# Kernel optimization log

Hardware: AMD Instinct MI355X
Metric: run time of the kernel (lower is better)

The kernel has to match this reference:

```python
import jax, jax.numpy as jnp
import numpy as np

B, L, T = 256, 256, 50  # batch, max_len, num_tags


def setup_inputs() -> dict:
    key = jax.random.key(0)
    k1, k2, k3 = jax.random.split(key, 3)
    feats = jax.random.normal(k1, (B, L, T), dtype=jnp.float32)
    trans_m = jax.random.normal(k2, (T, T), dtype=jnp.float32)
    tags = jax.random.randint(k3, (B, L), 0, T)
    mask = jnp.ones((B, L), dtype=jnp.int32)
    return {"feats": feats, "trans_m": trans_m, "tags": tags, "mask": mask}


def _normalizer(logits, trans_m, m):
    # logits: (L, B, T), m: (L, B) float mask
    alpha0 = logits[0]  # (B, T)

    def step(alpha, inp):
        emit, mt = inp  # (B, T), (B,)
        # (B, T_from, T_to) broadcast add, logsumexp over T_from
        tmp = alpha[:, :, None] + trans_m[None, :, :] + emit[:, None, :]
        new = jax.nn.logsumexp(tmp, axis=1)
        alpha = jnp.where(mt[:, None] > 0, new, alpha)
        return alpha, None

    alpha, _ = jax.lax.scan(step, alpha0, (logits[1:], m[1:]))
    return jax.nn.logsumexp(alpha, axis=1)  # (B,)


def _gold_score(logits, trans_m, tags_t, m):
    # logits: (L, B, T); tags_t: (L, B); m: (L, B)
    trans_sc = trans_m[tags_t[:-1], tags_t[1:]] * m[1:]  # (L-1, B)
    emit_sc = jnp.take_along_axis(logits, tags_t[:, :, None], axis=2)[..., 0] * m  # (L, B)
    return jnp.sum(trans_sc + emit_sc[:-1], axis=0) + emit_sc[-1]  # (B,)


def reference(feats, trans_m, tags, mask):
    # feats: (B, L, T) -> (L, B, T); include_start_end_trans=False
    logits = jnp.transpose(feats, (1, 0, 2))
    tags_t = tags.T
    m = mask.T.astype(feats.dtype)
    all_path = _normalizer(logits, trans_m, m)
    gold = _gold_score(logits, trans_m, tags_t, m)
    return all_path - gold  # (B,) loss per example
```

## Files before the change

kernel.cpp:

```cpp
#include <hip/hip_runtime.h>
#include <math.h>


#define TAGS 50
#define LEN 256
#define NB 256
#define HALF 128
#define INV_LN2 1.4426950408889634f
#define LN2 0.6931471805599453f

typedef __attribute__((ext_vector_type(8))) short bf16x8;
typedef __attribute__((ext_vector_type(4))) float f32x4;

#if __has_builtin(__builtin_amdgcn_exp2f)
#define EXP2F(x) __builtin_amdgcn_exp2f(x)
#else
#define EXP2F(x) exp2f(x)
#endif
#if __has_builtin(__builtin_amdgcn_logf)
#define LOG2F(x) __builtin_amdgcn_logf(x)
#else
#define LOG2F(x) log2f(x)
#endif
#if __has_builtin(__builtin_amdgcn_rcpf)
#define RCPF(x) __builtin_amdgcn_rcpf(x)
#else
#define RCPF(x) (1.0f / (x))
#endif

__device__ __forceinline__ float readlane_f(float v, int srclane) {
  return __builtin_bit_cast(float,
      __builtin_amdgcn_readlane(__builtin_bit_cast(int, v), srclane));
}

__device__ __forceinline__ int bf16pair(float lo, float hi) {
  unsigned lb = (__builtin_bit_cast(unsigned, lo) + 0x8000u) >> 16;
  unsigned hb = (__builtin_bit_cast(unsigned, hi) + 0x8000u) & 0xFFFF0000u;
  return (int)(hb | lb);
}

union U8 { int i[4]; bf16x8 v; };

#define WS_U(b)  ((b) * 64)
#define WS_W(b)  ((NB + (b)) * 64)
#define WS_SF(b) (2 * NB * 64 + (b))
#define WS_SB(b) (2 * NB * 64 + NB + (b))

__global__ __launch_bounds__(64) void crf_scan_kernel(
    const float* __restrict__ feats,
    const float* __restrict__ trans,
    const int*   __restrict__ mask,
    float*       __restrict__ ws)
{
  const int bid    = blockIdx.x;
  const bool is_fwd = bid < NB;
  const int b      = is_fwd ? bid : bid - NB;
  const int lane   = threadIdx.x;
  const int q      = lane >> 4;
  const int n      = lane & 15;

  __shared__ __align__(16) float fraw[HALF * TAGS];
  __shared__ __align__(16) float flexp[HALF * 64];
  __shared__ int ml[HALF];

  const int base_l = is_fwd ? 0 : HALF;
  const float* fb = feats + ((size_t)b * LEN + base_l) * TAGS;
  const int*   mb = mask + b * LEN + base_l;

  {
    const float4* fv = (const float4*)fb;
    for (int i = lane; i < (HALF * TAGS) / 4; i += 64) {
      float4 v4 = fv[i];
      v4.x *= INV_LN2; v4.y *= INV_LN2; v4.z *= INV_LN2; v4.w *= INV_LN2;
      *(float4*)&fraw[i * 4] = v4;
    }
    for (int i = lane; i < HALF; i += 64) ml[i] = mb[i];
  }
  __syncthreads();

  for (int l = 0; l < HALF; ++l) {
    float v = 0.0f;
    if (lane < TAGS) v = EXP2F(fraw[l * TAGS + lane]);
    flexp[l * 64 + lane] = v;
  }
  __syncthreads();

  U8 Afr[4][2];
#pragma unroll
  for (int t = 0; t < 4; ++t)
#pragma unroll
    for (int c = 0; c < 2; ++c)
#pragma unroll
      for (int r = 0; r < 4; ++r) {
        const int col = 16 * t + n;
        const int tag0 = 16 * c + 4 * q + r;
        const int tag1 = tag0 + 32;
        float e0 = 0.0f, e1 = 0.0f;
        if (col < TAGS) {
          if (tag0 < TAGS)
            e0 = EXP2F((is_fwd ? trans[tag0 * TAGS + col]
                               : trans[col * TAGS + tag0]) * INV_LN2);
          if (tag1 < TAGS)
            e1 = EXP2F((is_fwd ? trans[tag1 * TAGS + col]
                               : trans[col * TAGS + tag1]) * INV_LN2);
        }
        Afr[t][c].i[r] = bf16pair(e0, e1);
      }

  const f32x4 zero4 = {0.0f, 0.0f, 0.0f, 0.0f};

#define LDEH(l_, I_) (*(const f32x4*)&flexp[(l_) * 64 + 16 * (I_) + 4 * q])

  float va[16];
  float S;

  if (is_fwd) {
    const float r0 = RCPF(flexp[0]);
    {
      f32x4 i0 = LDEH(0, 0), i1 = LDEH(0, 1), i2 = LDEH(0, 2), i3 = LDEH(0, 3);
#pragma unroll
      for (int r = 0; r < 4; ++r) {
        va[r]      = i0[r] * r0;
        va[4 + r]  = i1[r] * r0;
        va[8 + r]  = i2[r] * r0;
        va[12 + r] = i3[r] * r0;
      }
    }
    S = fraw[0];

    f32x4 eh0 = LDEH(1, 0), eh1 = LDEH(1, 1), eh2 = LDEH(1, 2), eh3 = LDEH(1, 3);
    int m_nxt = ml[1];

#pragma unroll 2
    for (int l = 1; l < HALF; ++l) {
      const int m_cur = m_nxt;
      const int ln = (l + 1 < HALF) ? (l + 1) : (HALF - 1);

      const float cc = readlane_f(va[0], 0);
      const float rr = RCPF(cc);

      U8 B0, B1;
#pragma unroll
      for (int r = 0; r < 4; ++r) {
        B0.i[r] = bf16pair(va[r],     va[8 + r]);
        B1.i[r] = bf16pair(va[4 + r], va[12 + r]);
      }

      f32x4 d0 = __builtin_amdgcn_mfma_f32_16x16x32_bf16(Afr[0][1].v, B1.v, zero4, 0, 0, 0);
      f32x4 d1 = __builtin_amdgcn_mfma_f32_16x16x32_bf16(Afr[1][1].v, B1.v, zero4, 0, 0, 0);
      f32x4 d2 = __builtin_amdgcn_mfma_f32_16x16x32_bf16(Afr[2][1].v, B1.v, zero4, 0, 0, 0);
      f32x4 d3 = __builtin_amdgcn_mfma_f32_16x16x32_bf16(Afr[3][1].v, B1.v, zero4, 0, 0, 0);
      d0 = __builtin_amdgcn_mfma_f32_16x16x32_bf16(Afr[0][0].v, B0.v, d0, 0, 0, 0);
      d1 = __builtin_amdgcn_mfma_f32_16x16x32_bf16(Afr[1][0].v, B0.v, d1, 0, 0, 0);
      d2 = __builtin_amdgcn_mfma_f32_16x16x32_bf16(Afr[2][0].v, B0.v, d2, 0, 0, 0);
      d3 = __builtin_amdgcn_mfma_f32_16x16x32_bf16(Afr[3][0].v, B0.v, d3, 0, 0, 0);

      f32x4 en0 = LDEH(ln, 0), en1 = LDEH(ln, 1), en2 = LDEH(ln, 2), en3 = LDEH(ln, 3);
      const int m_n2 = ml[ln];

#pragma unroll
      for (int r = 0; r < 4; ++r) {
        va[r]      = ((m_cur > 0) ? d0[r] * eh0[r] : va[r])      * rr;
        va[4 + r]  = ((m_cur > 0) ? d1[r] * eh1[r] : va[4 + r])  * rr;
        va[8 + r]  = ((m_cur > 0) ? d2[r] * eh2[r] : va[8 + r])  * rr;
        va[12 + r] = ((m_cur > 0) ? d3[r] * eh3[r] : va[12 + r]) * rr;
      }
      S += LOG2F(cc);
      eh0 = en0; eh1 = en1; eh2 = en2; eh3 = en3;
      m_nxt = m_n2;
    }

    if (n == 0) {
#pragma unroll
      for (int I = 0; I < 4; ++I)
#pragma unroll
        for (int r = 0; r < 4; ++r)
          ws[WS_U(b) + 16 * I + 4 * q + r] = va[4 * I + r];
    }
    if (lane == 0) ws[WS_SF(b)] = S;
  } else {
#pragma unroll
    for (int I = 0; I < 4; ++I)
#pragma unroll
      for (int r = 0; r < 4; ++r)
        va[4 * I + r] = (16 * I + 4 * q + r < TAGS) ? 1.0f : 0.0f;
    S = 0.0f;

    f32x4 eh0 = LDEH(HALF - 1, 0), eh1 = LDEH(HALF - 1, 1),
          eh2 = LDEH(HALF - 1, 2), eh3 = LDEH(HALF - 1, 3);
    int m_nxt = ml[HALF - 1];

#pragma unroll 2
    for (int l = HALF - 1; l >= 0; --l) {
      const int m_cur = m_nxt;
      const int ln = (l > 0) ? (l - 1) : 0;

      const float cc = readlane_f(va[0], 0);
      const float rr = RCPF(cc);

      float x[16];
#pragma unroll
      for (int r = 0; r < 4; ++r) {
        x[r]      = va[r]      * eh0[r];
        x[4 + r]  = va[4 + r]  * eh1[r];
        x[8 + r]  = va[8 + r]  * eh2[r];
        x[12 + r] = va[12 + r] * eh3[r];
      }

      U8 B0, B1;
#pragma unroll
      for (int r = 0; r < 4; ++r) {
        B0.i[r] = bf16pair(x[r],     x[8 + r]);
        B1.i[r] = bf16pair(x[4 + r], x[12 + r]);
      }

      f32x4 d0 = __builtin_amdgcn_mfma_f32_16x16x32_bf16(Afr[0][1].v, B1.v, zero4, 0, 0, 0);
      f32x4 d1 = __builtin_amdgcn_mfma_f32_16x16x32_bf16(Afr[1][1].v, B1.v, zero4, 0, 0, 0);
      f32x4 d2 = __builtin_amdgcn_mfma_f32_16x16x32_bf16(Afr[2][1].v, B1.v, zero4, 0, 0, 0);
      f32x4 d3 = __builtin_amdgcn_mfma_f32_16x16x32_bf16(Afr[3][1].v, B1.v, zero4, 0, 0, 0);
      d0 = __builtin_amdgcn_mfma_f32_16x16x32_bf16(Afr[0][0].v, B0.v, d0, 0, 0, 0);
      d1 = __builtin_amdgcn_mfma_f32_16x16x32_bf16(Afr[1][0].v, B0.v, d1, 0, 0, 0);
      d2 = __builtin_amdgcn_mfma_f32_16x16x32_bf16(Afr[2][0].v, B0.v, d2, 0, 0, 0);
      d3 = __builtin_amdgcn_mfma_f32_16x16x32_bf16(Afr[3][0].v, B0.v, d3, 0, 0, 0);

      f32x4 en0 = LDEH(ln, 0), en1 = LDEH(ln, 1), en2 = LDEH(ln, 2), en3 = LDEH(ln, 3);
      const int m_n2 = ml[ln];

#pragma unroll
      for (int r = 0; r < 4; ++r) {
        va[r]      = ((m_cur > 0) ? d0[r] : va[r])      * rr;
        va[4 + r]  = ((m_cur > 0) ? d1[r] : va[4 + r])  * rr;
        va[8 + r]  = ((m_cur > 0) ? d2[r] : va[8 + r])  * rr;
        va[12 + r] = ((m_cur > 0) ? d3[r] : va[12 + r]) * rr;
      }
      S += LOG2F(cc);
      eh0 = en0; eh1 = en1; eh2 = en2; eh3 = en3;
      m_nxt = m_n2;
    }

    if (n == 0) {
#pragma unroll
      for (int I = 0; I < 4; ++I)
#pragma unroll
        for (int r = 0; r < 4; ++r)
          ws[WS_W(b) + 16 * I + 4 * q + r] = va[4 * I + r];
    }
    if (lane == 0) ws[WS_SB(b)] = S;
  }
#undef LDEH
}

__global__ __launch_bounds__(64) void crf_combine_kernel(
    const float* __restrict__ feats,
    const float* __restrict__ trans,
    const int*   __restrict__ tags,
    const int*   __restrict__ mask,
    const float* __restrict__ ws,
    float*       __restrict__ out)
{
  const int b = blockIdx.x;
  const int lane = threadIdx.x;

  float s = ws[WS_U(b) + lane] * ws[WS_W(b) + lane];
#pragma unroll
  for (int off = 32; off; off >>= 1) s += __shfl_xor(s, off, 64);

  const float* fb = feats + (size_t)b * (LEN * TAGS);
  const int*   tb = tags + b * LEN;
  const int*   mb = mask + b * LEN;
  float gp = 0.0f;
#pragma unroll
  for (int k = 0; k < 4; ++k) {
    const int p = lane + 64 * k;
    const int tg = tb[p];
    if (mb[p] > 0) {
      float vv = fb[p * TAGS + tg];
      if (p >= 1) vv += trans[tb[p - 1] * TAGS + tg];
      gp += vv;
    }
  }
#pragma unroll
  for (int off = 32; off; off >>= 1) gp += __shfl_xor(gp, off, 64);

  if (lane == 0) {
    const float Sf = ws[WS_SF(b)];
    const float Sb = ws[WS_SB(b)];
    out[b] = LN2 * (Sf + Sb + LOG2F(s)) - gp;
  }
}

extern "C" void kernel_launch(void* const* d_in, const int* in_sizes, int n_in,
                              void* d_out, int out_size, void* d_ws, size_t ws_size,
                              hipStream_t stream) {
  const float* feats = (const float*)d_in[0];
  const float* trans = (const float*)d_in[1];
  const int*   tags  = (const int*)d_in[2];
  const int*   mask  = (const int*)d_in[3];
  float* out = (float*)d_out;
  float* ws  = (float*)d_ws;

  crf_scan_kernel<<<2 * NB, 64, 0, stream>>>(feats, trans, mask, ws);
  crf_combine_kernel<<<NB, 64, 0, stream>>>(feats, trans, tags, mask, ws, out);
}
```

Measured before the change: 116.8 us.

## Split CRF scan into eight parallel segment transfer-matrix products per batch

Replaces the forward/backward two-kernel scheme with a single 512-thread block per sequence. Each of eight waves computes a 32-step segment transfer matrix (64x64) with MFMA, and the segments are then chained on one wave through LDS as vector-matrix products. The gold-path score is computed in the same block, so the workspace round trip and the second launch go away. The cost is 4x more MFMA work per step, since each step now multiplies a full matrix instead of a vector. The intermediate matrices are also stored in bf16, which may reduce accuracy.

```diff
diff --git a/kernel.cpp b/kernel.cpp
--- a/kernel.cpp
+++ b/kernel.cpp
@@ -5,12 +5,13 @@
 #define TAGS 50
 #define LEN 256
 #define NB 256
-#define HALF 128
+#define TOTF (NB * LEN * TAGS)
 #define INV_LN2 1.4426950408889634f
 #define LN2 0.6931471805599453f
 
 typedef __attribute__((ext_vector_type(8))) short bf16x8;
 typedef __attribute__((ext_vector_type(4))) float f32x4;
+typedef __attribute__((ext_vector_type(4), aligned(4))) float f32x4u;
 
 #if __has_builtin(__builtin_amdgcn_exp2f)
 #define EXP2F(x) __builtin_amdgcn_exp2f(x)
@@ -33,57 +34,49 @@
       __builtin_amdgcn_readlane(__builtin_bit_cast(int, v), srclane));
 }
 
-__device__ __forceinline__ int bf16pair(float lo, float hi) {
+__device__ __forceinline__ int bf16pairInit(float lo, float hi) {
   unsigned lb = (__builtin_bit_cast(unsigned, lo) + 0x8000u) >> 16;
   unsigned hb = (__builtin_bit_cast(unsigned, hi) + 0x8000u) & 0xFFFF0000u;
   return (int)(hb | lb);
 }
 
+__device__ __forceinline__ float bf16f(unsigned short u) {
+  return __builtin_bit_cast(float, ((unsigned)u) << 16);
+}
+
+#define PACK2(dst, lo, hi) \
+  asm("v_cvt_pk_bf16_f32 %0, %1, %2" : "=v"(dst) : "v"(lo), "v"(hi))
+
 union U8 { int i[4]; bf16x8 v; };
 
-#define WS_U(b)  ((b) * 64)
-#define WS_W(b)  ((NB + (b)) * 64)
-#define WS_SF(b) (2 * NB * 64 + (b))
-#define WS_SB(b) (2 * NB * 64 + NB + (b))
-
-__global__ __launch_bounds__(64) void crf_scan_kernel(
+__global__ __launch_bounds__(512, 1) void crf_seg_kernel(
     const float* __restrict__ feats,
     const float* __restrict__ trans,
+    const int*   __restrict__ tags,
     const int*   __restrict__ mask,
-    float*       __restrict__ ws)
+    float*       __restrict__ out)
 {
-  const int bid    = blockIdx.x;
-  const bool is_fwd = bid < NB;
-  const int b      = is_fwd ? bid : bid - NB;
-  const int lane   = threadIdx.x;
-  const int q      = lane >> 4;
-  const int n      = lane & 15;
-
-  __shared__ __align__(16) float fraw[HALF * TAGS];
-  __shared__ __align__(16) float flexp[HALF * 64];
-  __shared__ int ml[HALF];
-
-  const int base_l = is_fwd ? 0 : HALF;
-  const float* fb = feats + ((size_t)b * LEN + base_l) * TAGS;
-  const int*   mb = mask + b * LEN + base_l;
-
-  {
-    const float4* fv = (const float4*)fb;
-    for (int i = lane; i < (HALF * TAGS) / 4; i += 64) {
-      float4 v4 = fv[i];
-      v4.x *= INV_LN2; v4.y *= INV_LN2; v4.z *= INV_LN2; v4.w *= INV_LN2;
-      *(float4*)&fraw[i * 4] = v4;
-    }
-    for (int i = lane; i < HALF; i += 64) ml[i] = mb[i];
-  }
-  __syncthreads();
-
-  for (int l = 0; l < HALF; ++l) {
-    float v = 0.0f;
-    if (lane < TAGS) v = EXP2F(fraw[l * TAGS + lane]);
-    flexp[l * 64 + lane] = v;
-  }
-  __syncthreads();
+  const int b    = blockIdx.x;
+  const int tid  = threadIdx.x;
+  const int w    = tid >> 6;
+  const int lane = tid & 63;
+  const int q    = lane >> 4;
+  const int n    = lane & 15;
+
+  __shared__ __align__(16) unsigned short Plds[6][64][64];
+  __shared__ __align__(16) float u_lds[64];
+  __shared__ __align__(16) float w_lds[64];
+  __shared__ float Sseg[8];
+  __shared__ float norm_s, gold_s;
+
+  const int* mbp = mask + b * LEN;
+  const unsigned long long mb0 = __ballot(mbp[lane] > 0);
+  const unsigned long long mb1 = __ballot(mbp[64 + lane] > 0);
+  const unsigned long long mb2 = __ballot(mbp[128 + lane] > 0);
+  const unsigned long long mb3 = __ballot(mbp[192 + lane] > 0);
+#define MASKBIT(L)                                                          \
+  ((int)(((((L) & 128) ? (((L) & 64) ? mb3 : mb2)                           \
+                       : (((L) & 64) ? mb1 : mb0)) >> ((L) & 63)) & 1ull))
 
   U8 Afr[4][2];
 #pragma unroll
@@ -97,196 +90,218 @@
         const int tag1 = tag0 + 32;
         float e0 = 0.0f, e1 = 0.0f;
         if (col < TAGS) {
-          if (tag0 < TAGS)
-            e0 = EXP2F((is_fwd ? trans[tag0 * TAGS + col]
-                               : trans[col * TAGS + tag0]) * INV_LN2);
-          if (tag1 < TAGS)
-            e1 = EXP2F((is_fwd ? trans[tag1 * TAGS + col]
-                               : trans[col * TAGS + tag1]) * INV_LN2);
+          if (tag0 < TAGS) e0 = EXP2F(trans[tag0 * TAGS + col] * INV_LN2);
+          if (tag1 < TAGS) e1 = EXP2F(trans[tag1 * TAGS + col] * INV_LN2);
         }
-        Afr[t][c].i[r] = bf16pair(e0, e1);
+        Afr[t][c].i[r] = bf16pairInit(e0, e1);
       }
 
   const f32x4 zero4 = {0.0f, 0.0f, 0.0f, 0.0f};
 
-#define LDEH(l_, I_) (*(const f32x4*)&flexp[(l_) * 64 + 16 * (I_) + 4 * q])
-
-  float va[16];
-  float S;
-
-  if (is_fwd) {
-    const float r0 = RCPF(flexp[0]);
-    {
-      f32x4 i0 = LDEH(0, 0), i1 = LDEH(0, 1), i2 = LDEH(0, 2), i3 = LDEH(0, 3);
-#pragma unroll
-      for (int r = 0; r < 4; ++r) {
-        va[r]      = i0[r] * r0;
-        va[4 + r]  = i1[r] * r0;
-        va[8 + r]  = i2[r] * r0;
-        va[12 + r] = i3[r] * r0;
+  f32x4 d[4][4];
+#pragma unroll
+  for (int J = 0; J < 4; ++J)
+#pragma unroll
+    for (int I = 0; I < 4; ++I)
+#pragma unroll
+      for (int r = 0; r < 4; ++r)
+        d[J][I][r] = (16 * J + n == 16 * I + 4 * q + r) ? 1.0f : 0.0f;
+
+  const int l0 = 32 * w + 1;
+  float S = 0.0f;
+  f32x4u rA[4], rB[4];
+
+#define LOADG(BK, L) do {                                                   \
+    const float* _p = feats + (size_t)b * (LEN * TAGS) + (size_t)(L) * TAGS;\
+    BK[0] = *(const f32x4u*)(_p + 4 * q);                                   \
+    BK[1] = *(const f32x4u*)(_p + 16 + 4 * q);                              \
+    BK[2] = *(const f32x4u*)(_p + 32 + 4 * q);                              \
+    const float* _p3 = _p + 46 + 4 * q;                                     \
+    const float* _lim = feats + (TOTF - 4);                                 \
+    if (_p3 > _lim) _p3 = _lim;                                             \
+    BK[3] = *(const f32x4u*)_p3;                                            \
+  } while (0)
+
+#define RENORMM() do {                                                      \
+    const float _cc = readlane_f(d[0][0][0], 0);                            \
+    const float _rr = RCPF(_cc);                                            \
+    S += LOG2F(_cc);                                                        \
+    _Pragma("unroll") for (int _J = 0; _J < 4; ++_J)                        \
+    _Pragma("unroll") for (int _I = 0; _I < 4; ++_I)                        \
+    _Pragma("unroll") for (int _r = 0; _r < 4; ++_r)                        \
+      d[_J][_I][_r] *= _rr;                                                 \
+  } while (0)
+
+#define STEPM(EH, L) do {                                                   \
+    if (MASKBIT(L)) {                                                       \
+      float ev[4][4];                                                       \
+      _Pragma("unroll") for (int _i = 0; _i < 3; ++_i)                      \
+      _Pragma("unroll") for (int _r = 0; _r < 4; ++_r)                      \
+        ev[_i][_r] = EXP2F(EH[_i][_r] * INV_LN2);                           \
+      ev[3][0] = EXP2F(EH[3][2] * INV_LN2);                                 \
+      ev[3][1] = EXP2F(EH[3][3] * INV_LN2);                                 \
+      ev[3][2] = 0.0f; ev[3][3] = 0.0f;                                     \
+      _Pragma("unroll") for (int _J = 0; _J < 4; ++_J) {                    \
+        U8 B0, B1;                                                          \
+        _Pragma("unroll") for (int _r = 0; _r < 4; ++_r) {                  \
+          PACK2(B0.i[_r], d[_J][0][_r], d[_J][2][_r]);                      \
+          PACK2(B1.i[_r], d[_J][1][_r], d[_J][3][_r]);                      \
+        }                                                                   \
+        f32x4 t0 = __builtin_amdgcn_mfma_f32_16x16x32_bf16(Afr[0][1].v, B1.v, zero4, 0, 0, 0); \
+        f32x4 t1 = __builtin_amdgcn_mfma_f32_16x16x32_bf16(Afr[1][1].v, B1.v, zero4, 0, 0, 0); \
+        f32x4 t2 = __builtin_amdgcn_mfma_f32_16x16x32_bf16(Afr[2][1].v, B1.v, zero4, 0, 0, 0); \
+        f32x4 t3 = __builtin_amdgcn_mfma_f32_16x16x32_bf16(Afr[3][1].v, B1.v, zero4, 0, 0, 0); \
+        t0 = __builtin_amdgcn_mfma_f32_16x16x32_bf16(Afr[0][0].v, B0.v, t0, 0, 0, 0); \
+        t1 = __builtin_amdgcn_mfma_f32_16x16x32_bf16(Afr[1][0].v, B0.v, t1, 0, 0, 0); \
+        t2 = __builtin_amdgcn_mfma_f32_16x16x32_bf16(Afr[2][0].v, B0.v, t2, 0, 0, 0); \
+        t3 = __builtin_amdgcn_mfma_f32_16x16x32_bf16(Afr[3][0].v, B0.v, t3, 0, 0, 0); \
+        _Pragma("unroll") for (int _r = 0; _r < 4; ++_r) {                  \
+          d[_J][0][_r] = t0[_r] * ev[0][_r];                                \
+          d[_J][1][_r] = t1[_r] * ev[1][_r];                                \
+          d[_J][2][_r] = t2[_r] * ev[2][_r];                                \
+          d[_J][3][_r] = t3[_r] * ev[3][_r];                                \
+        }                                                                   \
+      }                                                                     \
+    }                                                                       \
+  } while (0)
+
+  LOADG(rA, l0);
+  LOADG(rB, l0 + 1);
+
+  for (int k = 0; k < 15; ++k) {
+    const int l = l0 + 2 * k;
+    if ((k & 1) == 0) RENORMM();
+    STEPM(rA, l);
+    { const int rl = (l + 2 < 255) ? l + 2 : 255; LOADG(rA, rl); }
+    STEPM(rB, l + 1);
+    { const int rl = (l + 3 < 255) ? l + 3 : 255; LOADG(rB, rl); }
+  }
+  STEPM(rA, l0 + 30);
+  if (w != 7) STEPM(rB, l0 + 31);
+
+  if (lane == 0) Sseg[w] = S;
+
+  if (w == 0) {
+    float v0v[4];
+#pragma unroll
+    for (int J = 0; J < 4; ++J) {
+      const int tg = 16 * J + n;
+      const float f = feats[(size_t)b * (LEN * TAGS) + tg];
+      v0v[J] = (tg < TAGS) ? EXP2F(f * INV_LN2) : 0.0f;
+    }
+    float pu[4][4];
+#pragma unroll
+    for (int I = 0; I < 4; ++I)
+#pragma unroll
+      for (int r = 0; r < 4; ++r)
+        pu[I][r] = v0v[0] * d[0][I][r] + v0v[1] * d[1][I][r] +
+                   v0v[2] * d[2][I][r] + v0v[3] * d[3][I][r];
+#pragma unroll
+    for (int off = 1; off <= 8; off <<= 1)
+#pragma unroll
+      for (int I = 0; I < 4; ++I)
+#pragma unroll
+        for (int r = 0; r < 4; ++r)
+          pu[I][r] += __shfl_xor(pu[I][r], off, 64);
+    if (n == 0) {
+#pragma unroll
+      for (int I = 0; I < 4; ++I)
+#pragma unroll
+        for (int r = 0; r < 4; ++r)
+          u_lds[16 * I + 4 * q + r] = pu[I][r];
+    }
+  } else if (w == 7) {
+    float pw[4];
+#pragma unroll
+    for (int J = 0; J < 4; ++J) {
+      float s = 0.0f;
+#pragma unroll
+      for (int I = 0; I < 4; ++I)
+#pragma unroll
+        for (int r = 0; r < 4; ++r)
+          s += d[J][I][r];
+      pw[J] = s;
+    }
+#pragma unroll
+    for (int J = 0; J < 4; ++J) {
+      pw[J] += __shfl_xor(pw[J], 16, 64);
+      pw[J] += __shfl_xor(pw[J], 32, 64);
+    }
+    if (q == 0) {
+#pragma unroll
+      for (int J = 0; J < 4; ++J) w_lds[16 * J + n] = pw[J];
+    }
+  } else {
+#pragma unroll
+    for (int J = 0; J < 4; ++J)
+#pragma unroll
+      for (int I = 0; I < 4; ++I) {
+        int lo, hi;
+        PACK2(lo, d[J][I][0], d[J][I][1]);
+        PACK2(hi, d[J][I][2], d[J][I][3]);
+        unsigned* dst = (unsigned*)&Plds[w - 1][16 * J + n][16 * I + 4 * q];
+        dst[0] = (unsigned)lo;
+        dst[1] = (unsigned)hi;
       }
-    }
-    S = fraw[0];
-
-    f32x4 eh0 = LDEH(1, 0), eh1 = LDEH(1, 1), eh2 = LDEH(1, 2), eh3 = LDEH(1, 3);
-    int m_nxt = ml[1];
-
-#pragma unroll 2
-    for (int l = 1; l < HALF; ++l) {
-      const int m_cur = m_nxt;
-      const int ln = (l + 1 < HALF) ? (l + 1) : (HALF - 1);
-
-      const float cc = readlane_f(va[0], 0);
-      const float rr = RCPF(cc);
-
-      U8 B0, B1;
-#pragma unroll
-      for (int r = 0; r < 4; ++r) {
-        B0.i[r] = bf16pair(va[r],     va[8 + r]);
-        B1.i[r] = bf16pair(va[4 + r], va[12 + r]);
+  }
+
+  __syncthreads();
+
+  if (w == 0) {
+    float x = u_lds[lane];
+    float stot = 0.0f;
+    for (int j = 0; j < 6; ++j) {
+      u_lds[lane] = x;
+      asm volatile("s_waitcnt lgkmcnt(0)" ::: "memory");
+      float y0 = 0.0f, y1 = 0.0f, y2 = 0.0f, y3 = 0.0f;
+#pragma unroll 4
+      for (int r = 0; r < 64; r += 4) {
+        y0 += u_lds[r]     * bf16f(Plds[j][r][lane]);
+        y1 += u_lds[r + 1] * bf16f(Plds[j][r + 1][lane]);
+        y2 += u_lds[r + 2] * bf16f(Plds[j][r + 2][lane]);
+        y3 += u_lds[r + 3] * bf16f(Plds[j][r + 3][lane]);
       }
-
-      f32x4 d0 = __builtin_amdgcn_mfma_f32_16x16x32_bf16(Afr[0][1].v, B1.v, zero4, 0, 0, 0);
-      f32x4 d1 = __builtin_amdgcn_mfma_f32_16x16x32_bf16(Afr[1][1].v, B1.v, zero4, 0, 0, 0);
-      f32x4 d2 = __builtin_amdgcn_mfma_f32_16x16x32_bf16(Afr[2][1].v, B1.v, zero4, 0, 0, 0);
-      f32x4 d3 = __builtin_amdgcn_mfma_f32_16x16x32_bf16(Afr[3][1].v, B1.v, zero4, 0, 0, 0);
-      d0 = __builtin_amdgcn_mfma_f32_16x16x32_bf16(Afr[0][0].v, B0.v, d0, 0, 0, 0);
-      d1 = __builtin_amdgcn_mfma_f32_16x16x32_bf16(Afr[1][0].v, B0.v, d1, 0, 0, 0);
-      d2 = __builtin_amdgcn_mfma_f32_16x16x32_bf16(Afr[2][0].v, B0.v, d2, 0, 0, 0);
-      d3 = __builtin_amdgcn_mfma_f32_16x16x32_bf16(Afr[3][0].v, B0.v, d3, 0, 0, 0);
-
-      f32x4 en0 = LDEH(ln, 0), en1 = LDEH(ln, 1), en2 = LDEH(ln, 2), en3 = LDEH(ln, 3);
-      const int m_n2 = ml[ln];
-
-#pragma unroll
-      for (int r = 0; r < 4; ++r) {
-        va[r]      = ((m_cur > 0) ? d0[r] * eh0[r] : va[r])      * rr;
-        va[4 + r]  = ((m_cur > 0) ? d1[r] * eh1[r] : va[4 + r])  * rr;
-        va[8 + r]  = ((m_cur > 0) ? d2[r] * eh2[r] : va[8 + r])  * rr;
-        va[12 + r] = ((m_cur > 0) ? d3[r] * eh3[r] : va[12 + r]) * rr;
+      float y = (y0 + y1) + (y2 + y3);
+      const float cc = readlane_f(y, 0);
+      stot += LOG2F(cc);
+      x = y * RCPF(cc);
+      asm volatile("s_waitcnt lgkmcnt(0)" ::: "memory");
+    }
+    float dotv = x * w_lds[lane];
+#pragma unroll
+    for (int off = 32; off; off >>= 1) dotv += __shfl_xor(dotv, off, 64);
+    if (lane == 0) {
+      float Ssum = 0.0f;
+#pragma unroll
+      for (int i = 0; i < 8; ++i) Ssum += Sseg[i];
+      norm_s = LN2 * (Ssum + stot + LOG2F(dotv));
+    }
+  } else if (w == 1) {
+    const float* fb = feats + (size_t)b * (LEN * TAGS);
+    const int* tb = tags + b * LEN;
+    float gp = 0.0f;
+#pragma unroll
+    for (int k = 0; k < 4; ++k) {
+      const int p = lane + 64 * k;
+      const int tg = tb[p];
+      if (mbp[p] > 0) {
+        float vv = fb[p * TAGS + tg];
+        if (p >= 1) vv += trans[tb[p - 1] * TAGS + tg];
+        gp += vv;
       }
-      S += LOG2F(cc);
-      eh0 = en0; eh1 = en1; eh2 = en2; eh3 = en3;
-      m_nxt = m_n2;
-    }
-
-    if (n == 0) {
-#pragma unroll
-      for (int I = 0; I < 4; ++I)
-#pragma unroll
-        for (int r = 0; r < 4; ++r)
-          ws[WS_U(b) + 16 * I + 4 * q + r] = va[4 * I + r];
-    }
-    if (lane == 0) ws[WS_SF(b)] = S;
-  } else {
-#pragma unroll
-    for (int I = 0; I < 4; ++I)
-#pragma unroll
-      for (int r = 0; r < 4; ++r)
-        va[4 * I + r] = (16 * I + 4 * q + r < TAGS) ? 1.0f : 0.0f;
-    S = 0.0f;
-
-    f32x4 eh0 = LDEH(HALF - 1, 0), eh1 = LDEH(HALF - 1, 1),
-          eh2 = LDEH(HALF - 1, 2), eh3 = LDEH(HALF - 1, 3);
-    int m_nxt = ml[HALF - 1];
-
-#pragma unroll 2
-    for (int l = HALF - 1; l >= 0; --l) {
-      const int m_cur = m_nxt;
-      const int ln = (l > 0) ? (l - 1) : 0;
-
-      const float cc = readlane_f(va[0], 0);
-      const float rr = RCPF(cc);
-
-      float x[16];
-#pragma unroll
-      for (int r = 0; r < 4; ++r) {
-        x[r]      = va[r]      * eh0[r];
-        x[4 + r]  = va[4 + r]  * eh1[r];
-        x[8 + r]  = va[8 + r]  * eh2[r];
-        x[12 + r] = va[12 + r] * eh3[r];
-      }
-
-      U8 B0, B1;
-#pragma unroll
-      for (int r = 0; r < 4; ++r) {
-        B0.i[r] = bf16pair(x[r],     x[8 + r]);
-        B1.i[r] = bf16pair(x[4 + r], x[12 + r]);
-      }
-
-      f32x4 d0 = __builtin_amdgcn_mfma_f32_16x16x32_bf16(Afr[0][1].v, B1.v, zero4, 0, 0, 0);
-      f32x4 d1 = __builtin_amdgcn_mfma_f32_16x16x32_bf16(Afr[1][1].v, B1.v, zero4, 0, 0, 0);
-      f32x4 d2 = __builtin_amdgcn_mfma_f32_16x16x32_bf16(Afr[2][1].v, B1.v, zero4, 0, 0, 0);
-      f32x4 d3 = __builtin_amdgcn_mfma_f32_16x16x32_bf16(Afr[3][1].v, B1.v, zero4, 0, 0, 0);
-      d0 = __builtin_amdgcn_mfma_f32_16x16x32_bf16(Afr[0][0].v, B0.v, d0, 0, 0, 0);
-      d1 = __builtin_amdgcn_mfma_f32_16x16x32_bf16(Afr[1][0].v, B0.v, d1, 0, 0, 0);
-      d2 = __builtin_amdgcn_mfma_f32_16x16x32_bf16(Afr[2][0].v, B0.v, d2, 0, 0, 0);
-      d3 = __builtin_amdgcn_mfma_f32_16x16x32_bf16(Afr[3][0].v, B0.v, d3, 0, 0, 0);
-
-      f32x4 en0 = LDEH(ln, 0), en1 = LDEH(ln, 1), en2 = LDEH(ln, 2), en3 = LDEH(ln, 3);
-      const int m_n2 = ml[ln];
-
-#pragma unroll
-      for (int r = 0; r < 4; ++r) {
-        va[r]      = ((m_cur > 0) ? d0[r] : va[r])      * rr;
-        va[4 + r]  = ((m_cur > 0) ? d1[r] : va[4 + r])  * rr;
-        va[8 + r]  = ((m_cur > 0) ? d2[r] : va[8 + r])  * rr;
-        va[12 + r] = ((m_cur > 0) ? d3[r] : va[12 + r]) * rr;
-      }
-      S += LOG2F(cc);
-      eh0 = en0; eh1 = en1; eh2 = en2; eh3 = en3;
-      m_nxt = m_n2;
-    }
-
-    if (n == 0) {
-#pragma unroll
-      for (int I = 0; I < 4; ++I)
-#pragma unroll
-        for (int r = 0; r < 4; ++r)
-          ws[WS_W(b) + 16 * I + 4 * q + r] = va[4 * I + r];
-    }
-    if (lane == 0) ws[WS_SB(b)] = S;
+    }
+#pragma unroll
+    for (int off = 32; off; off >>= 1) gp += __shfl_xor(gp, off, 64);
+    if (lane == 0) gold_s = gp;
   }
-#undef LDEH
-}
-
-__global__ __launch_bounds__(64) void crf_combine_kernel(
-    const float* __restrict__ feats,
-    const float* __restrict__ trans,
-    const int*   __restrict__ tags,
-    const int*   __restrict__ mask,
-    const float* __restrict__ ws,
-    float*       __restrict__ out)
-{
-  const int b = blockIdx.x;
-  const int lane = threadIdx.x;
-
-  float s = ws[WS_U(b) + lane] * ws[WS_W(b) + lane];
-#pragma unroll
-  for (int off = 32; off; off >>= 1) s += __shfl_xor(s, off, 64);
-
-  const float* fb = feats + (size_t)b * (LEN * TAGS);
-  const int*   tb = tags + b * LEN;
-  const int*   mb = mask + b * LEN;
-  float gp = 0.0f;
-#pragma unroll
-  for (int k = 0; k < 4; ++k) {
-    const int p = lane + 64 * k;
-    const int tg = tb[p];
-    if (mb[p] > 0) {
-      float vv = fb[p * TAGS + tg];
-      if (p >= 1) vv += trans[tb[p - 1] * TAGS + tg];
-      gp += vv;
-    }
-  }
-#pragma unroll
-  for (int off = 32; off; off >>= 1) gp += __shfl_xor(gp, off, 64);
-
-  if (lane == 0) {
-    const float Sf = ws[WS_SF(b)];
-    const float Sb = ws[WS_SB(b)];
-    out[b] = LN2 * (Sf + Sb + LOG2F(s)) - gp;
-  }
+
+  __syncthreads();
+  if (tid == 0) out[b] = norm_s - gold_s;
+
+#undef MASKBIT
+#undef LOADG
+#undef RENORMM
+#undef STEPM
 }
 
 extern "C" void kernel_launch(void* const* d_in, const int* in_sizes, int n_in,
@@ -297,8 +312,7 @@
   const int*   tags  = (const int*)d_in[2];
   const int*   mask  = (const int*)d_in[3];
   float* out = (float*)d_out;
-  float* ws  = (float*)d_ws;
-
-  crf_scan_kernel<<<2 * NB, 64, 0, stream>>>(feats, trans, mask, ws);
-  crf_combine_kernel<<<NB, 64, 0, stream>>>(feats, trans, tags, mask, ws, out);
-}
+  (void)d_ws; (void)ws_size;
+
+  crf_seg_kernel<<<NB, 512, 0, stream>>>(feats, trans, tags, mask, out);
+}
```

Measured after the change: 106.1 us. 9.1% less time.
